# Kernel optimization log

Hardware: AMD Instinct MI355X
Metric: run time of the kernel (lower is better)

The kernel has to match this reference:

```python
import jax, jax.numpy as jnp
import numpy as np

B, S, D = 2, 2048, 1024
H, DH = 16, 64          # n_heads, size_per_head; H*DH == D
FF = 4096               # hidden_dim
EPS = 1e-6              # flax LayerNorm default


def _layernorm(x, scale, bias):
    mu = jnp.mean(x, axis=-1, keepdims=True)
    var = jnp.mean(jnp.square(x - mu), axis=-1, keepdims=True)
    return (x - mu) * jax.lax.rsqrt(var + EPS) * scale + bias


def setup_inputs() -> dict:
    key = jax.random.key(0)
    ks = jax.random.split(key, 12)
    p = lambda k, shape: (jax.random.normal(k, shape, dtype=jnp.float32) * 0.02)
    return {
        "X": jax.random.normal(ks[0], (B, S, D), dtype=jnp.float32),
        "mask": jax.random.randint(ks[1], (B, S), 0, 2, dtype=jnp.int32),
        "Wq": p(ks[2], (D, H * DH)), "bq": jnp.zeros((H * DH,), jnp.float32),
        "Wk": p(ks[3], (D, H * DH)), "bk": jnp.zeros((H * DH,), jnp.float32),
        "Wv": p(ks[4], (D, H * DH)), "bv": jnp.zeros((H * DH,), jnp.float32),
        "Wo": p(ks[5], (H * DH, D)), "bo": jnp.zeros((D,), jnp.float32),
        "ln0_scale": jnp.ones((D,), jnp.float32), "ln0_bias": jnp.zeros((D,), jnp.float32),
        "W1": p(ks[6], (D, FF)), "b1": jnp.zeros((FF,), jnp.float32),
        "W2": p(ks[7], (FF, D)), "b2": jnp.zeros((D,), jnp.float32),
        "ln1_scale": jnp.ones((D,), jnp.float32), "ln1_bias": jnp.zeros((D,), jnp.float32),
    }


def reference(X, mask, Wq, bq, Wk, bk, Wv, bv, Wo, bo,
              ln0_scale, ln0_bias, W1, b1, W2, b2, ln1_scale, ln1_bias):
    b, n, d = X.shape

    def proj(x, W, bias):
        # (B,S,D) -> (B,H,S,DH)
        return (x @ W + bias).reshape(b, n, H, DH).swapaxes(1, 2)

    q = proj(X, Wq, bq)
    k = proj(X, Wk, bk)
    v = proj(X, Wv, bv)

    # scaled dot-product attention with additive padding mask
    scores = jnp.einsum('bhnd,bhmd->bhnm', q, k) / jnp.sqrt(jnp.asarray(DH, X.dtype))
    m = mask[:, None, None, :].astype(scores.dtype)  # (B,1,1,M)
    scores = scores + m * -10000.0
    attn = jax.nn.softmax(scores, axis=-1)
    out = jnp.einsum('bhnm,bhmd->bhnd', attn, v)      # (B,H,S,DH)
    out = out.swapaxes(1, 2).reshape(b, n, H * DH)
    out = out @ Wo + bo

    # add & norm
    X1 = _layernorm(X + out, ln0_scale, ln0_bias)

    # feed-forward
    ff = jnp.maximum(X1 @ W1 + b1, 0.0) @ W2 + b2

    # add & norm
    return _layernorm(X1 + ff, ln1_scale, ln1_bias)
```

## Files before the change

### kernel.cpp

```cpp
#include <hip/hip_runtime.h>
#include <hip/hip_bf16.h>
#include <stdint.h>

#define B_ 2
#define S_ 2048
#define D_ 1024
#define H_ 16
#define DH_ 64
#define FF_ 4096
#define M_ (B_*S_)

typedef __bf16 bf16;
typedef __bf16 bf16x4 __attribute__((ext_vector_type(4)));
typedef __bf16 bf16x8 __attribute__((ext_vector_type(8)));
typedef float f32x4 __attribute__((ext_vector_type(4)));

#define LOG2E 1.44269504f

__device__ __forceinline__ float fexp2(float x) {
#if __has_builtin(__builtin_amdgcn_exp2f)
  return __builtin_amdgcn_exp2f(x);
#else
  return exp2f(x);
#endif
}

__device__ __forceinline__ void gload_lds16(const void* g, void* l) {
  auto gp = reinterpret_cast<const __attribute__((address_space(1))) void*>(
      reinterpret_cast<uintptr_t>(g));
  auto lp = reinterpret_cast<__attribute__((address_space(3))) void*>(
      reinterpret_cast<uintptr_t>(l));
  __builtin_amdgcn_global_load_lds(gp, lp, 16, 0, 0);
}

__global__ __launch_bounds__(256) void prep_all(
    const float* __restrict__ X, bf16* __restrict__ Xb,
    const float* __restrict__ bq, const float* __restrict__ bk,
    const float* __restrict__ bv, float* __restrict__ bqkv,
    const int* __restrict__ mask, float* __restrict__ Mp,
    const float* __restrict__ Wq, const float* __restrict__ Wk,
    const float* __restrict__ Wv, const float* __restrict__ Wo,
    const float* __restrict__ W1, const float* __restrict__ W2,
    bf16* __restrict__ Wqkvt, bf16* __restrict__ Wot,
    bf16* __restrict__ W1t, bf16* __restrict__ W2t) {
  int bid = blockIdx.x;
  const int tid = threadIdx.x;
  if (bid < 4096) {
    int i = (bid * 256 + tid) * 4;
    float4 v = *(const float4*)(X + i);
    Xb[i+0] = (bf16)v.x; Xb[i+1] = (bf16)v.y;
    Xb[i+2] = (bf16)v.z; Xb[i+3] = (bf16)v.w;
    return;
  }
  bid -= 4096;
  if (bid < 12) {
    int i = bid * 256 + tid;
    bqkv[i] = i < 1024 ? bq[i] : (i < 2048 ? bk[i-1024] : bv[i-2048]);
    return;
  }
  bid -= 12;
  if (bid < 16) {
    int i = bid * 256 + tid;
    Mp[i] = (-10000.0f * LOG2E) * (float)mask[i];
    return;
  }
  bid -= 16;
  const float* src; bf16* dst; int K, N;
  if (bid < 1024)      { src = Wq; dst = Wqkvt;                     K=1024; N=1024; }
  else if (bid < 2048) { src = Wk; dst = Wqkvt + (size_t)1024*1024; K=1024; N=1024; bid -= 1024; }
  else if (bid < 3072) { src = Wv; dst = Wqkvt + (size_t)2048*1024; K=1024; N=1024; bid -= 2048; }
  else if (bid < 4096) { src = Wo; dst = Wot;                       K=1024; N=1024; bid -= 3072; }
  else if (bid < 8192) { src = W1; dst = W1t;                       K=1024; N=4096; bid -= 4096; }
  else                 { src = W2; dst = W2t;                       K=4096; N=1024; bid -= 8192; }
  __shared__ float t[32][33];
  const int tx = tid & 31, ty = tid >> 5;
  const int nt32 = N >> 5;
  const int n0 = (bid % nt32) * 32, k0 = (bid / nt32) * 32;
#pragma unroll
  for (int i = 0; i < 4; i++)
    t[ty + i*8][tx] = src[(size_t)(k0 + ty + i*8) * N + n0 + tx];
  __syncthreads();
#pragma unroll
  for (int i = 0; i < 4; i++)
    dst[(size_t)(n0 + ty + i*8) * K + k0 + tx] = (bf16)t[tx][ty + i*8];
}
#define PREP_BLOCKS (4096 + 12 + 16 + 4*1024 + 2*4096)

__global__ __launch_bounds__(256) void transpose_v(
    const bf16* __restrict__ QKV, bf16* __restrict__ Vt) {
  __shared__ bf16 t[64][66];
  int bh = blockIdx.x, s0 = blockIdx.y * 64;
  int b = bh >> 4, h = bh & 15;
  int w = threadIdx.x >> 6, l = threadIdx.x & 63;
#pragma unroll
  for (int i = 0; i < 16; i++) {
    int sr = w*16 + i;
    t[sr][l] = QKV[(size_t)(b*S_ + s0 + sr) * 3072 + 2*D_ + h*DH_ + l];
  }
  __syncthreads();
  const int pcol = (l & 15) * 4 + (l >> 4);
#pragma unroll
  for (int i = 0; i < 16; i++) {
    int dh = w*16 + i;
    Vt[((size_t)(bh*DH_ + dh)) * S_ + s0 + pcol] = t[l][dh];
  }
}

template<int SK>
__global__ __launch_bounds__(256) void gemm_sk(
    const bf16* __restrict__ A, const bf16* __restrict__ Bt,
    const float* __restrict__ bias, float* __restrict__ Cp,
    int M, int N, int K) {
  __shared__ bf16 As[2][128*64];
  __shared__ bf16 Bs[2][128*64];
  const int tid = threadIdx.x;
  const int w = tid >> 6, l = tid & 63;
  const int wm = w >> 1, wn = w & 1;
  const int r16 = l & 15, g = l >> 4;

  const int gx = gridDim.x, gxy = gx * gridDim.y;
  const int nwg = gxy * SK;
  const int lid = (blockIdx.z * gridDim.y + blockIdx.y) * gx + blockIdx.x;
  const int swz = (lid & 7) * (nwg >> 3) + (lid >> 3);
  const int z = swz / gxy, rem = swz % gxy;
  const int m0 = (rem / gx) * 128, n0 = (rem % gx) * 128;
  const int kc = K / SK, kb = z * kc;

  const int srow = w*8 + (l >> 3);
  const int sch  = ((l & 7) ^ (l >> 3)) * 8;
  const bf16* ag = A + (size_t)(m0 + srow) * K + kb + sch;
  const bf16* bg = Bt + (size_t)(n0 + srow) * K + kb + sch;

  f32x4 acc[4][4];
#pragma unroll
  for (int i = 0; i < 4; i++)
#pragma unroll
    for (int j = 0; j < 4; j++) acc[i][j] = (f32x4){0.f,0.f,0.f,0.f};

#pragma unroll
  for (int q = 0; q < 4; q++) {
    gload_lds16(ag + (size_t)(q*32) * K, &As[0][(q*32 + w*8) * 64]);
    gload_lds16(bg + (size_t)(q*32) * K, &Bs[0][(q*32 + w*8) * 64]);
  }
  asm volatile("s_waitcnt vmcnt(0)" ::: "memory");
  __builtin_amdgcn_s_barrier();
  asm volatile("" ::: "memory");

  const int nt = kc >> 6;
  int cur = 0;
  for (int t = 0; t < nt; ++t) {
    if (t + 1 < nt) {
      const int k0 = (t + 1) * 64;
#pragma unroll
      for (int q = 0; q < 4; q++) {
        gload_lds16(ag + (size_t)(q*32) * K + k0, &As[cur^1][(q*32 + w*8) * 64]);
        gload_lds16(bg + (size_t)(q*32) * K + k0, &Bs[cur^1][(q*32 + w*8) * 64]);
      }
    }
    bf16x8 af[4][2], bfr[4][2];
#pragma unroll
    for (int mi = 0; mi < 4; mi++)
#pragma unroll
      for (int kk = 0; kk < 2; kk++) {
        const int row = wm*64 + mi*16 + r16;
        af[mi][kk] = *(const bf16x8*)&As[cur][row*64 + (((kk*4+g) ^ (row & 7)))*8];
      }
#pragma unroll
    for (int ni = 0; ni < 4; ni++)
#pragma unroll
      for (int kk = 0; kk < 2; kk++) {
        const int row = wn*64 + ni*16 + r16;
        bfr[ni][kk] = *(const bf16x8*)&Bs[cur][row*64 + (((kk*4+g) ^ (row & 7)))*8];
      }
    __builtin_amdgcn_s_setprio(1);
#pragma unroll
    for (int mi = 0; mi < 4; mi++)
#pragma unroll
      for (int ni = 0; ni < 4; ni++)
#pragma unroll
        for (int kk = 0; kk < 2; kk++)
          acc[mi][ni] = __builtin_amdgcn_mfma_f32_16x16x32_bf16(
              af[mi][kk], bfr[ni][kk], acc[mi][ni], 0, 0, 0);
    __builtin_amdgcn_s_setprio(0);

    asm volatile("s_waitcnt vmcnt(0)" ::: "memory");
    __builtin_amdgcn_s_barrier();
    asm volatile("" ::: "memory");
    cur ^= 1;
  }

  float* outp = Cp + (size_t)z * M * N;
  float bvs[4];
#pragma unroll
  for (int ni = 0; ni < 4; ni++)
    bvs[ni] = (z == 0) ? bias[n0 + wn*64 + ni*16 + r16] : 0.f;
#pragma unroll
  for (int mi = 0; mi < 4; mi++)
#pragma unroll
    for (int ni = 0; ni < 4; ni++)
#pragma unroll
      for (int r = 0; r < 4; r++) {
        size_t row = (size_t)(m0 + wm*64 + mi*16 + g*4 + r);
        size_t col = (size_t)(n0 + wn*64 + ni*16 + r16);
        outp[row * N + col] = acc[mi][ni][r] + bvs[ni];
      }
}

template<bool RELU>
__global__ __launch_bounds__(512) void gemm256(
    const bf16* __restrict__ A, const bf16* __restrict__ Bt,
    const float* __restrict__ bias, bf16* __restrict__ C,
    int M, int N, int K) {
  __shared__ bf16 As[2][256*64];
  __shared__ bf16 Bs[2][256*64];
  const int tid = threadIdx.x;
  const int w = tid >> 6, l = tid & 63;
  const int wm = w >> 2, wn = w & 3;
  const int r16 = l & 15, g = l >> 4;

  const int gx = gridDim.x;
  const int nwg = gx * gridDim.y;
  const int lid = blockIdx.y * gx + blockIdx.x;
  const int swz = (lid & 7) * (nwg >> 3) + (lid >> 3);
  const int m0 = (swz / gx) * 256, n0 = (swz % gx) * 256;

  const int srow = w*8 + (l >> 3);
  const int sch  = ((l & 7) ^ (l >> 3)) * 8;
  const bf16* ag = A  + (size_t)(m0 + srow) * K + sch;
  const bf16* bg = Bt + (size_t)(n0 + srow) * K + sch;

  f32x4 acc[8][4];
#pragma unroll
  for (int i = 0; i < 8; i++)
#pragma unroll
    for (int j = 0; j < 4; j++) acc[i][j] = (f32x4){0.f,0.f,0.f,0.f};

#pragma unroll
  for (int q = 0; q < 4; q++) {
    gload_lds16(ag + (size_t)(q*64) * K, &As[0][(q*64 + w*8) * 64]);
    gload_lds16(bg + (size_t)(q*64) * K, &Bs[0][(q*64 + w*8) * 64]);
  }
  asm volatile("s_waitcnt vmcnt(0)" ::: "memory");
  __builtin_amdgcn_s_barrier();
  asm volatile("" ::: "memory");

  const int nt = K >> 6;
  int cur = 0;
  for (int t = 0; t < nt; ++t) {
    if (t + 1 < nt) {
      const size_t k0 = (size_t)(t + 1) << 6;
#pragma unroll
      for (int q = 0; q < 4; q++) {
        gload_lds16(ag + (size_t)(q*64) * K + k0, &As[cur^1][(q*64 + w*8) * 64]);
        gload_lds16(bg + (size_t)(q*64) * K + k0, &Bs[cur^1][(q*64 + w*8) * 64]);
      }
    }

    bf16x8 af[4][2], blo[2][2], bhi[2][2];
#pragma unroll
    for (int mi = 0; mi < 4; mi++)
#pragma unroll
      for (int kk = 0; kk < 2; kk++) {
        const int row = wm*128 + mi*16 + r16;
        af[mi][kk] = *(const bf16x8*)&As[cur][row*64 + (((kk*4+g) ^ (row & 7)))*8];
      }
#pragma unroll
    for (int ni = 0; ni < 2; ni++)
#pragma unroll
      for (int kk = 0; kk < 2; kk++) {
        const int row = wn*64 + ni*16 + r16;
        blo[ni][kk] = *(const bf16x8*)&Bs[cur][row*64 + (((kk*4+g) ^ (row & 7)))*8];
      }
    __builtin_amdgcn_s_setprio(1);
#pragma unroll
    for (int mi = 0; mi < 4; mi++)
#pragma unroll
      for (int ni = 0; ni < 2; ni++)
#pragma unroll
        for (int kk = 0; kk < 2; kk++)
          acc[mi][ni] = __builtin_amdgcn_mfma_f32_16x16x32_bf16(
              af[mi][kk], blo[ni][kk], acc[mi][ni], 0, 0, 0);
    __builtin_amdgcn_s_setprio(0);
#pragma unroll
    for (int ni = 0; ni < 2; ni++)
#pragma unroll
      for (int kk = 0; kk < 2; kk++) {
        const int row = wn*64 + 32 + ni*16 + r16;
        bhi[ni][kk] = *(const bf16x8*)&Bs[cur][row*64 + (((kk*4+g) ^ (row & 7)))*8];
      }
    __builtin_amdgcn_s_setprio(1);
#pragma unroll
    for (int mi = 0; mi < 4; mi++)
#pragma unroll
      for (int ni = 0; ni < 2; ni++)
#pragma unroll
        for (int kk = 0; kk < 2; kk++)
          acc[mi][2+ni] = __builtin_amdgcn_mfma_f32_16x16x32_bf16(
              af[mi][kk], bhi[ni][kk], acc[mi][2+ni], 0, 0, 0);
    __builtin_amdgcn_s_setprio(0);
#pragma unroll
    for (int mi = 0; mi < 4; mi++)
#pragma unroll
      for (int kk = 0; kk < 2; kk++) {
        const int row = wm*128 + 64 + mi*16 + r16;
        af[mi][kk] = *(const bf16x8*)&As[cur][row*64 + (((kk*4+g) ^ (row & 7)))*8];
      }
    __builtin_amdgcn_s_setprio(1);
#pragma unroll
    for (int mi = 0; mi < 4; mi++)
#pragma unroll
      for (int ni = 0; ni < 2; ni++)
#pragma unroll
        for (int kk = 0; kk < 2; kk++)
          acc[4+mi][2+ni] = __builtin_amdgcn_mfma_f32_16x16x32_bf16(
              af[mi][kk], bhi[ni][kk], acc[4+mi][2+ni], 0, 0, 0);
    __builtin_amdgcn_s_setprio(0);
    __builtin_amdgcn_s_setprio(1);
#pragma unroll
    for (int mi = 0; mi < 4; mi++)
#pragma unroll
      for (int ni = 0; ni < 2; ni++)
#pragma unroll
        for (int kk = 0; kk < 2; kk++)
          acc[4+mi][ni] = __builtin_amdgcn_mfma_f32_16x16x32_bf16(
              af[mi][kk], blo[ni][kk], acc[4+mi][ni], 0, 0, 0);
    __builtin_amdgcn_s_setprio(0);

    asm volatile("s_waitcnt vmcnt(0)" ::: "memory");
    __builtin_amdgcn_s_barrier();
    asm volatile("" ::: "memory");
    cur ^= 1;
  }

  float bvs[4];
#pragma unroll
  for (int ni = 0; ni < 4; ni++) bvs[ni] = bias[n0 + wn*64 + ni*16 + r16];
#pragma unroll
  for (int mi = 0; mi < 8; mi++)
#pragma unroll
    for (int ni = 0; ni < 4; ni++)
#pragma unroll
      for (int r = 0; r < 4; r++) {
        float v = acc[mi][ni][r] + bvs[ni];
        if (RELU) v = fmaxf(v, 0.f);
        C[(size_t)(m0 + wm*128 + mi*16 + g*4 + r) * N +
          (n0 + wn*64 + ni*16 + r16)] = (bf16)v;
      }
}

__global__ __launch_bounds__(256) void attn(
    const bf16* __restrict__ QKV, const bf16* __restrict__ Vt,
    const float* __restrict__ Mp, bf16* __restrict__ AO) {
  __shared__ bf16 Ks[2][64*64];
  __shared__ bf16 Vs[2][64*64];
  __shared__ bf16 Ps[4][32*72];

  const float SC2 = 0.125f * LOG2E;
  const int bh = blockIdx.x, b = bh >> 4, h = bh & 15;
  const int q0 = blockIdx.y * 128;
  const int tid = threadIdx.x, w = tid >> 6, l = tid & 63;
  const int r16 = l & 15, g = l >> 4;
  const int qw = q0 + w*32;

  bf16x8 qf[2][2];
#pragma unroll
  for (int s = 0; s < 2; s++)
#pragma unroll
    for (int kk = 0; kk < 2; kk++)
      qf[s][kk] = *(const bf16x8*)&QKV[((size_t)(b*S_ + qw + s*16 + r16))*3072
                                       + h*64 + kk*32 + g*8];

  const int srow = w*8 + (l >> 3);
  const int sch  = (l & 7) ^ (l >> 3);
  const bf16* kg = QKV + ((size_t)(b*S_) + srow)*3072 + 1024 + h*64 + sch*8;
  const bf16* vg = Vt + ((size_t)(bh*64 + srow))*S_ + sch*8;

  f32x4 po[2][4];
#pragma unroll
  for (int s = 0; s < 2; s++)
#pragma unroll
    for (int n = 0; n < 4; n++) po[s][n] = (f32x4){0.f,0.f,0.f,0.f};
  float mrun[8], lsum[8];
#pragma unroll
  for (int r = 0; r < 8; r++) { mrun[r] = -1.0e30f; lsum[r] = 0.f; }

  float madd[4];
#pragma unroll
  for (int ct = 0; ct < 4; ct++) madd[ct] = Mp[b*S_ + ct*16 + r16];
#pragma unroll
  for (int p = 0; p < 2; p++) {
    gload_lds16(kg + (size_t)(p*32)*3072, &Ks[0][(p*256 + w*64)*8]);
    gload_lds16(vg + (size_t)(p*32)*S_,   &Vs[0][(p*256 + w*64)*8]);
  }

  const int NT = S_/64;
  int cur = 0;
  for (int it = 0; it < NT; ++it) {
    const int kv0 = it * 64;
    if (it + 1 < NT) {
#pragma unroll
      for (int p = 0; p < 2; p++) {
        gload_lds16(kg + (size_t)(kv0 + 64 + p*32)*3072, &Ks[cur^1][(p*256 + w*64)*8]);
        gload_lds16(vg + (size_t)(p*32)*S_ + (kv0 + 64), &Vs[cur^1][(p*256 + w*64)*8]);
      }
      asm volatile("s_waitcnt vmcnt(4)" ::: "memory");
    } else {
      asm volatile("s_waitcnt vmcnt(0)" ::: "memory");
    }
    __builtin_amdgcn_s_barrier();
    asm volatile("" ::: "memory");

    float sv[2][4][4];
    __builtin_amdgcn_s_setprio(1);
#pragma unroll
    for (int ct = 0; ct < 4; ct++) {
      const int row = ct*16 + r16;
      bf16x8 kf0 = *(const bf16x8*)&Ks[cur][row*64 + ((g) ^ (row & 7))*8];
      bf16x8 kf1 = *(const bf16x8*)&Ks[cur][row*64 + ((4+g) ^ (row & 7))*8];
      f32x4 a0 = (f32x4){0.f,0.f,0.f,0.f}, a1 = (f32x4){0.f,0.f,0.f,0.f};
      a0 = __builtin_amdgcn_mfma_f32_16x16x32_bf16(qf[0][0], kf0, a0, 0, 0, 0);
      a0 = __builtin_amdgcn_mfma_f32_16x16x32_bf16(qf[0][1], kf1, a0, 0, 0, 0);
      a1 = __builtin_amdgcn_mfma_f32_16x16x32_bf16(qf[1][0], kf0, a1, 0, 0, 0);
      a1 = __builtin_amdgcn_mfma_f32_16x16x32_bf16(qf[1][1], kf1, a1, 0, 0, 0);
#pragma unroll
      for (int r = 0; r < 4; r++) {
        sv[0][ct][r] = a0[r]*SC2 + madd[ct];
        sv[1][ct][r] = a1[r]*SC2 + madd[ct];
      }
    }
    __builtin_amdgcn_s_setprio(0);

    if (it + 1 < NT) {
#pragma unroll
      for (int ct = 0; ct < 4; ct++)
        madd[ct] = Mp[b*S_ + kv0 + 64 + ct*16 + r16];
    }

    float lmax[8];
#pragma unroll
    for (int s = 0; s < 2; s++)
#pragma unroll
      for (int r = 0; r < 4; r++)
        lmax[s*4+r] = fmaxf(fmaxf(sv[s][0][r], sv[s][1][r]),
                            fmaxf(sv[s][2][r], sv[s][3][r]));
    bool grow = false;
#pragma unroll
    for (int i = 0; i < 8; i++) grow |= (lmax[i] > mrun[i] + 8.f);
    if (__any(grow)) {
#pragma unroll
      for (int s = 0; s < 2; s++)
#pragma unroll
        for (int r = 0; r < 4; r++) {
          const int i = s*4 + r;
          float t = lmax[i];
#pragma unroll
          for (int off = 8; off >= 1; off >>= 1) t = fmaxf(t, __shfl_xor(t, off, 16));
          float mnew = fmaxf(mrun[i], t);
          float sc = fexp2(mrun[i] - mnew);
          mrun[i] = mnew;
          lsum[i] *= sc;
#pragma unroll
          for (int n = 0; n < 4; n++) po[s][n][r] *= sc;
        }
    }
#pragma unroll
    for (int s = 0; s < 2; s++)
#pragma unroll
      for (int r = 0; r < 4; r++) {
        const int i = s*4 + r;
#pragma unroll
        for (int ct = 0; ct < 4; ct++)
          sv[s][ct][r] = fexp2(sv[s][ct][r] - mrun[i]);
        lsum[i] += (sv[s][0][r] + sv[s][1][r]) + (sv[s][2][r] + sv[s][3][r]);
      }

#pragma unroll
    for (int s = 0; s < 2; s++)
#pragma unroll
      for (int r = 0; r < 4; r++) {
        bf16x4 pk;
#pragma unroll
        for (int ct = 0; ct < 4; ct++) pk[ct] = (bf16)sv[s][ct][r];
        *(bf16x4*)&Ps[w][(s*16 + g*4 + r)*72 + r16*4] = pk;
      }
    asm volatile("s_waitcnt lgkmcnt(0)" ::: "memory");

    __builtin_amdgcn_s_setprio(1);
#pragma unroll
    for (int kk = 0; kk < 2; kk++) {
      bf16x8 pa0 = *(const bf16x8*)&Ps[w][(r16)*72 + kk*32 + g*8];
      bf16x8 pa1 = *(const bf16x8*)&Ps[w][(16 + r16)*72 + kk*32 + g*8];
#pragma unroll
      for (int n = 0; n < 4; n++) {
        const int row = n*16 + r16;
        bf16x8 vf = *(const bf16x8*)&Vs[cur][row*64 + ((kk*4 + g) ^ (row & 7))*8];
        po[0][n] = __builtin_amdgcn_mfma_f32_16x16x32_bf16(pa0, vf, po[0][n], 0, 0, 0);
        po[1][n] = __builtin_amdgcn_mfma_f32_16x16x32_bf16(pa1, vf, po[1][n], 0, 0, 0);
      }
    }
    __builtin_amdgcn_s_setprio(0);

    __builtin_amdgcn_s_barrier();
    asm volatile("" ::: "memory");
    cur ^= 1;
  }

#pragma unroll
  for (int i = 0; i < 8; i++) {
    float t = lsum[i];
#pragma unroll
    for (int off = 8; off >= 1; off >>= 1) t += __shfl_xor(t, off, 16);
    lsum[i] = t;
  }

#pragma unroll
  for (int s = 0; s < 2; s++)
#pragma unroll
    for (int n = 0; n < 4; n++)
#pragma unroll
      for (int r = 0; r < 4; r++) {
        float v = po[s][n][r] / lsum[s*4 + r];
        AO[(size_t)(b*S_ + qw + s*16 + g*4 + r)*D_ + h*64 + n*16 + r16] = (bf16)v;
      }
}

template<bool XF32, bool OUTF32>
__global__ __launch_bounds__(256) void ln_res2(
    const void* __restrict__ xp, const float* __restrict__ p0,
    const float* __restrict__ p1, const float* __restrict__ sc,
    const float* __restrict__ bi, float* __restrict__ y,
    bf16* __restrict__ yb) {
  const int row = blockIdx.x, tid = threadIdx.x;
  const size_t base = (size_t)row * D_;
  float v[4];
  if (XF32) {
    float4 a = ((const float4*)((const float*)xp + base))[tid];
    v[0] = a.x; v[1] = a.y; v[2] = a.z; v[3] = a.w;
  } else {
    bf16x4 a = *(const bf16x4*)&((const bf16*)xp)[base + tid*4];
#pragma unroll
    for (int j = 0; j < 4; j++) v[j] = (float)a[j];
  }
  float4 a0 = ((const float4*)(p0 + base))[tid];
  float4 a1 = ((const float4*)(p1 + base))[tid];
  v[0] += a0.x + a1.x; v[1] += a0.y + a1.y;
  v[2] += a0.z + a1.z; v[3] += a0.w + a1.w;
  float s  = v[0] + v[1] + v[2] + v[3];
  float ss = v[0]*v[0] + v[1]*v[1] + v[2]*v[2] + v[3]*v[3];
#pragma unroll
  for (int off = 32; off >= 1; off >>= 1) {
    s  += __shfl_xor(s, off, 64);
    ss += __shfl_xor(ss, off, 64);
  }
  __shared__ float red[8];
  const int wv = tid >> 6;
  if ((tid & 63) == 0) { red[wv] = s; red[4 + wv] = ss; }
  __syncthreads();
  s  = red[0] + red[1] + red[2] + red[3];
  ss = red[4] + red[5] + red[6] + red[7];
  const float mu  = s * (1.0f / D_);
  const float inv = rsqrtf(ss * (1.0f / D_) - mu*mu + 1e-6f);
  float4 scv = ((const float4*)sc)[tid];
  float4 biv = ((const float4*)bi)[tid];
  float o[4];
  o[0] = (v[0]-mu)*inv*scv.x + biv.x;
  o[1] = (v[1]-mu)*inv*scv.y + biv.y;
  o[2] = (v[2]-mu)*inv*scv.z + biv.z;
  o[3] = (v[3]-mu)*inv*scv.w + biv.w;
  if (OUTF32) {
    ((float4*)(y + base))[tid] = make_float4(o[0], o[1], o[2], o[3]);
  } else {
    bf16x4 ob;
#pragma unroll
    for (int j = 0; j < 4; j++) ob[j] = (bf16)o[j];
    *(bf16x4*)&yb[base + tid*4] = ob;
  }
}

extern "C" void kernel_launch(void* const* d_in, const int* in_sizes, int n_in,
                              void* d_out, int out_size, void* d_ws, size_t ws_size,
                              hipStream_t stream) {
  const float* X    = (const float*)d_in[0];
  const int*   mask = (const int*)d_in[1];
  const float* Wq   = (const float*)d_in[2];
  const float* bq   = (const float*)d_in[3];
  const float* Wk   = (const float*)d_in[4];
  const float* bk   = (const float*)d_in[5];
  const float* Wv   = (const float*)d_in[6];
  const float* bv   = (const float*)d_in[7];
  const float* Wo   = (const float*)d_in[8];
  const float* bo   = (const float*)d_in[9];
  const float* ln0s = (const float*)d_in[10];
  const float* ln0b = (const float*)d_in[11];
  const float* W1   = (const float*)d_in[12];
  const float* b1   = (const float*)d_in[13];
  const float* W2   = (const float*)d_in[14];
  const float* b2   = (const float*)d_in[15];
  const float* ln1s = (const float*)d_in[16];
  const float* ln1b = (const float*)d_in[17];
  float* out = (float*)d_out;

  char* ws = (char*)d_ws;
  const size_t MB = 1024 * 1024;
  bf16*  Xb    = (bf16*)(ws + 0);
  bf16*  X1b   = (bf16*)(ws + 0);
  bf16*  Wqkvt = (bf16*)(ws + 8*MB);
  bf16*  Wot   = (bf16*)(ws + 14*MB);
  bf16*  W1t   = (bf16*)(ws + 16*MB);
  bf16*  W2t   = (bf16*)(ws + 24*MB);
  bf16*  QKV   = (bf16*)(ws + 32*MB);
  bf16*  AO    = (bf16*)(ws + 32*MB);
  bf16*  Vt    = (bf16*)(ws + 56*MB);
  bf16*  FF1   = (bf16*)(ws + 32*MB);
  float* P0    = (float*)(ws + 64*MB);
  float* P1    = (float*)(ws + 80*MB);
  float* bqkv  = (float*)(ws + 64*MB);
  float* Mp    = (float*)(ws + 64*MB + 16384);

  prep_all<<<PREP_BLOCKS, 256, 0, stream>>>(
      X, Xb, bq, bk, bv, bqkv, mask, Mp,
      Wq, Wk, Wv, Wo, W1, W2, Wqkvt, Wot, W1t, W2t);

  gemm256<false><<<dim3(3072/256, M_/256), 512, 0, stream>>>(Xb, Wqkvt, bqkv, QKV, M_, 3072, D_);
  transpose_v<<<dim3(32, S_/64), 256, 0, stream>>>(QKV, Vt);
  attn<<<dim3(32, S_/128), 256, 0, stream>>>(QKV, Vt, Mp, AO);
  gemm_sk<2><<<dim3(D_/128, M_/128, 2), 256, 0, stream>>>(AO, Wot, bo, P0, M_, D_, D_);
  ln_res2<false,false><<<M_, 256, 0, stream>>>(Xb, P0, P1, ln0s, ln0b, nullptr, X1b);
  gemm256<true><<<dim3(FF_/256, M_/256), 512, 0, stream>>>(X1b, W1t, b1, FF1, M_, FF_, D_);
  gemm_sk<2><<<dim3(D_/128, M_/128, 2), 256, 0, stream>>>(FF1, W2t, b2, P0, M_, D_, FF_);
  ln_res2<false,true><<<M_, 256, 0, stream>>>(X1b, P0, P1, ln1s, ln1b, out, nullptr);
}
```

Baseline: 228.6 us.

## Split attention block into 8 waves of 16 query rows each

The attention kernel now launches 512 threads per block, with 8 waves each owning 16 query rows instead of 4 waves owning 32. K/V tile loads are spread over 8 waves, so each thread issues one load per tile instead of two. This is meant to raise wave-level parallelism and latency hiding and to cut per-wave registers. In exchange each wave reuses every K/V LDS fragment for only one MFMA, which doubles LDS read traffic per FLOP and adds barrier participants.

```diff
diff --git a/kernel.cpp b/kernel.cpp
--- a/kernel.cpp
+++ b/kernel.cpp
@@ -348,85 +348,70 @@
       }
 }
 
-__global__ __launch_bounds__(256) void attn(
+__global__ __launch_bounds__(512) void attn(
     const bf16* __restrict__ QKV, const bf16* __restrict__ Vt,
     const float* __restrict__ Mp, bf16* __restrict__ AO) {
   __shared__ bf16 Ks[2][64*64];
   __shared__ bf16 Vs[2][64*64];
-  __shared__ bf16 Ps[4][32*72];
+  __shared__ bf16 Ps[8][16*72];
 
   const float SC2 = 0.125f * LOG2E;
   const int bh = blockIdx.x, b = bh >> 4, h = bh & 15;
   const int q0 = blockIdx.y * 128;
   const int tid = threadIdx.x, w = tid >> 6, l = tid & 63;
   const int r16 = l & 15, g = l >> 4;
-  const int qw = q0 + w*32;
-
-  bf16x8 qf[2][2];
-#pragma unroll
-  for (int s = 0; s < 2; s++)
-#pragma unroll
-    for (int kk = 0; kk < 2; kk++)
-      qf[s][kk] = *(const bf16x8*)&QKV[((size_t)(b*S_ + qw + s*16 + r16))*3072
-                                       + h*64 + kk*32 + g*8];
+  const int qw = q0 + w*16;
+
+  bf16x8 qf[2];
+#pragma unroll
+  for (int kk = 0; kk < 2; kk++)
+    qf[kk] = *(const bf16x8*)&QKV[((size_t)(b*S_ + qw + r16))*3072
+                                  + h*64 + kk*32 + g*8];
 
   const int srow = w*8 + (l >> 3);
   const int sch  = (l & 7) ^ (l >> 3);
   const bf16* kg = QKV + ((size_t)(b*S_) + srow)*3072 + 1024 + h*64 + sch*8;
   const bf16* vg = Vt + ((size_t)(bh*64 + srow))*S_ + sch*8;
 
-  f32x4 po[2][4];
-#pragma unroll
-  for (int s = 0; s < 2; s++)
-#pragma unroll
-    for (int n = 0; n < 4; n++) po[s][n] = (f32x4){0.f,0.f,0.f,0.f};
-  float mrun[8], lsum[8];
-#pragma unroll
-  for (int r = 0; r < 8; r++) { mrun[r] = -1.0e30f; lsum[r] = 0.f; }
+  f32x4 po[4];
+#pragma unroll
+  for (int n = 0; n < 4; n++) po[n] = (f32x4){0.f,0.f,0.f,0.f};
+  float mrun[4], lsum[4];
+#pragma unroll
+  for (int r = 0; r < 4; r++) { mrun[r] = -1.0e30f; lsum[r] = 0.f; }
 
   float madd[4];
 #pragma unroll
   for (int ct = 0; ct < 4; ct++) madd[ct] = Mp[b*S_ + ct*16 + r16];
-#pragma unroll
-  for (int p = 0; p < 2; p++) {
-    gload_lds16(kg + (size_t)(p*32)*3072, &Ks[0][(p*256 + w*64)*8]);
-    gload_lds16(vg + (size_t)(p*32)*S_,   &Vs[0][(p*256 + w*64)*8]);
-  }
+  gload_lds16(kg, &Ks[0][w*512]);
+  gload_lds16(vg, &Vs[0][w*512]);
 
   const int NT = S_/64;
   int cur = 0;
   for (int it = 0; it < NT; ++it) {
     const int kv0 = it * 64;
     if (it + 1 < NT) {
-#pragma unroll
-      for (int p = 0; p < 2; p++) {
-        gload_lds16(kg + (size_t)(kv0 + 64 + p*32)*3072, &Ks[cur^1][(p*256 + w*64)*8]);
-        gload_lds16(vg + (size_t)(p*32)*S_ + (kv0 + 64), &Vs[cur^1][(p*256 + w*64)*8]);
-      }
-      asm volatile("s_waitcnt vmcnt(4)" ::: "memory");
+      gload_lds16(kg + (size_t)(kv0 + 64)*3072, &Ks[cur^1][w*512]);
+      gload_lds16(vg + kv0 + 64,                &Vs[cur^1][w*512]);
+      asm volatile("s_waitcnt vmcnt(2)" ::: "memory");
     } else {
       asm volatile("s_waitcnt vmcnt(0)" ::: "memory");
     }
     __builtin_amdgcn_s_barrier();
     asm volatile("" ::: "memory");
 
-    float sv[2][4][4];
+    float sv[4][4];
     __builtin_amdgcn_s_setprio(1);
 #pragma unroll
     for (int ct = 0; ct < 4; ct++) {
       const int row = ct*16 + r16;
       bf16x8 kf0 = *(const bf16x8*)&Ks[cur][row*64 + ((g) ^ (row & 7))*8];
       bf16x8 kf1 = *(const bf16x8*)&Ks[cur][row*64 + ((4+g) ^ (row & 7))*8];
-      f32x4 a0 = (f32x4){0.f,0.f,0.f,0.f}, a1 = (f32x4){0.f,0.f,0.f,0.f};
-      a0 = __builtin_amdgcn_mfma_f32_16x16x32_bf16(qf[0][0], kf0, a0, 0, 0, 0);
-      a0 = __builtin_amdgcn_mfma_f32_16x16x32_bf16(qf[0][1], kf1, a0, 0, 0, 0);
-      a1 = __builtin_amdgcn_mfma_f32_16x16x32_bf16(qf[1][0], kf0, a1, 0, 0, 0);
-      a1 = __builtin_amdgcn_mfma_f32_16x16x32_bf16(qf[1][1], kf1, a1, 0, 0, 0);
-#pragma unroll
-      for (int r = 0; r < 4; r++) {
-        sv[0][ct][r] = a0[r]*SC2 + madd[ct];
-        sv[1][ct][r] = a1[r]*SC2 + madd[ct];
-      }
+      f32x4 s = (f32x4){0.f,0.f,0.f,0.f};
+      s = __builtin_amdgcn_mfma_f32_16x16x32_bf16(qf[0], kf0, s, 0, 0, 0);
+      s = __builtin_amdgcn_mfma_f32_16x16x32_bf16(qf[1], kf1, s, 0, 0, 0);
+#pragma unroll
+      for (int r = 0; r < 4; r++) sv[ct][r] = s[r]*SC2 + madd[ct];
     }
     __builtin_amdgcn_s_setprio(0);
 
@@ -436,66 +421,52 @@
         madd[ct] = Mp[b*S_ + kv0 + 64 + ct*16 + r16];
     }
 
-    float lmax[8];
-#pragma unroll
-    for (int s = 0; s < 2; s++)
-#pragma unroll
-      for (int r = 0; r < 4; r++)
-        lmax[s*4+r] = fmaxf(fmaxf(sv[s][0][r], sv[s][1][r]),
-                            fmaxf(sv[s][2][r], sv[s][3][r]));
-    bool grow = false;
-#pragma unroll
-    for (int i = 0; i < 8; i++) grow |= (lmax[i] > mrun[i] + 8.f);
+    float lmax[4];
+#pragma unroll
+    for (int r = 0; r < 4; r++)
+      lmax[r] = fmaxf(fmaxf(sv[0][r], sv[1][r]), fmaxf(sv[2][r], sv[3][r]));
+    bool grow = (lmax[0] > mrun[0] + 8.f) | (lmax[1] > mrun[1] + 8.f) |
+                (lmax[2] > mrun[2] + 8.f) | (lmax[3] > mrun[3] + 8.f);
     if (__any(grow)) {
 #pragma unroll
-      for (int s = 0; s < 2; s++)
-#pragma unroll
-        for (int r = 0; r < 4; r++) {
-          const int i = s*4 + r;
-          float t = lmax[i];
-#pragma unroll
-          for (int off = 8; off >= 1; off >>= 1) t = fmaxf(t, __shfl_xor(t, off, 16));
-          float mnew = fmaxf(mrun[i], t);
-          float sc = fexp2(mrun[i] - mnew);
-          mrun[i] = mnew;
-          lsum[i] *= sc;
-#pragma unroll
-          for (int n = 0; n < 4; n++) po[s][n][r] *= sc;
-        }
-    }
-#pragma unroll
-    for (int s = 0; s < 2; s++)
-#pragma unroll
       for (int r = 0; r < 4; r++) {
-        const int i = s*4 + r;
-#pragma unroll
-        for (int ct = 0; ct < 4; ct++)
-          sv[s][ct][r] = fexp2(sv[s][ct][r] - mrun[i]);
-        lsum[i] += (sv[s][0][r] + sv[s][1][r]) + (sv[s][2][r] + sv[s][3][r]);
-      }
-
-#pragma unroll
-    for (int s = 0; s < 2; s++)
-#pragma unroll
-      for (int r = 0; r < 4; r++) {
-        bf16x4 pk;
-#pragma unroll
-        for (int ct = 0; ct < 4; ct++) pk[ct] = (bf16)sv[s][ct][r];
-        *(bf16x4*)&Ps[w][(s*16 + g*4 + r)*72 + r16*4] = pk;
-      }
+        float t = lmax[r];
+#pragma unroll
+        for (int off = 8; off >= 1; off >>= 1) t = fmaxf(t, __shfl_xor(t, off, 16));
+        float mnew = fmaxf(mrun[r], t);
+        float sc = fexp2(mrun[r] - mnew);
+        mrun[r] = mnew;
+        lsum[r] *= sc;
+#pragma unroll
+        for (int n = 0; n < 4; n++) po[n][r] *= sc;
+      }
+    }
+#pragma unroll
+    for (int r = 0; r < 4; r++) {
+#pragma unroll
+      for (int ct = 0; ct < 4; ct++)
+        sv[ct][r] = fexp2(sv[ct][r] - mrun[r]);
+      lsum[r] += (sv[0][r] + sv[1][r]) + (sv[2][r] + sv[3][r]);
+    }
+
+#pragma unroll
+    for (int r = 0; r < 4; r++) {
+      bf16x4 pk;
+#pragma unroll
+      for (int ct = 0; ct < 4; ct++) pk[ct] = (bf16)sv[ct][r];
+      *(bf16x4*)&Ps[w][(g*4 + r)*72 + r16*4] = pk;
+    }
     asm volatile("s_waitcnt lgkmcnt(0)" ::: "memory");
 
     __builtin_amdgcn_s_setprio(1);
 #pragma unroll
     for (int kk = 0; kk < 2; kk++) {
-      bf16x8 pa0 = *(const bf16x8*)&Ps[w][(r16)*72 + kk*32 + g*8];
-      bf16x8 pa1 = *(const bf16x8*)&Ps[w][(16 + r16)*72 + kk*32 + g*8];
+      bf16x8 pa = *(const bf16x8*)&Ps[w][r16*72 + kk*32 + g*8];
 #pragma unroll
       for (int n = 0; n < 4; n++) {
         const int row = n*16 + r16;
         bf16x8 vf = *(const bf16x8*)&Vs[cur][row*64 + ((kk*4 + g) ^ (row & 7))*8];
-        po[0][n] = __builtin_amdgcn_mfma_f32_16x16x32_bf16(pa0, vf, po[0][n], 0, 0, 0);
-        po[1][n] = __builtin_amdgcn_mfma_f32_16x16x32_bf16(pa1, vf, po[1][n], 0, 0, 0);
+        po[n] = __builtin_amdgcn_mfma_f32_16x16x32_bf16(pa, vf, po[n], 0, 0, 0);
       }
     }
     __builtin_amdgcn_s_setprio(0);
@@ -506,22 +477,20 @@
   }
 
 #pragma unroll
-  for (int i = 0; i < 8; i++) {
-    float t = lsum[i];
+  for (int r = 0; r < 4; r++) {
+    float t = lsum[r];
 #pragma unroll
     for (int off = 8; off >= 1; off >>= 1) t += __shfl_xor(t, off, 16);
-    lsum[i] = t;
-  }
-
-#pragma unroll
-  for (int s = 0; s < 2; s++)
-#pragma unroll
-    for (int n = 0; n < 4; n++)
-#pragma unroll
-      for (int r = 0; r < 4; r++) {
-        float v = po[s][n][r] / lsum[s*4 + r];
-        AO[(size_t)(b*S_ + qw + s*16 + g*4 + r)*D_ + h*64 + n*16 + r16] = (bf16)v;
-      }
+    lsum[r] = t;
+  }
+
+#pragma unroll
+  for (int n = 0; n < 4; n++)
+#pragma unroll
+    for (int r = 0; r < 4; r++) {
+      float v = po[n][r] / lsum[r];
+      AO[(size_t)(b*S_ + qw + g*4 + r)*D_ + h*64 + n*16 + r16] = (bf16)v;
+    }
 }
 
 template<bool XF32, bool OUTF32>
@@ -623,7 +592,7 @@
 
   gemm256<false><<<dim3(3072/256, M_/256), 512, 0, stream>>>(Xb, Wqkvt, bqkv, QKV, M_, 3072, D_);
   transpose_v<<<dim3(32, S_/64), 256, 0, stream>>>(QKV, Vt);
-  attn<<<dim3(32, S_/128), 256, 0, stream>>>(QKV, Vt, Mp, AO);
+  attn<<<dim3(32, S_/128), 512, 0, stream>>>(QKV, Vt, Mp, AO);
   gemm_sk<2><<<dim3(D_/128, M_/128, 2), 256, 0, stream>>>(AO, Wot, bo, P0, M_, D_, D_);
   ln_res2<false,false><<<M_, 256, 0, stream>>>(Xb, P0, P1, ln0s, ln0b, nullptr, X1b);
   gemm256<true><<<dim3(FF_/256, M_/256), 512, 0, stream>>>(X1b, W1t, b1, FF1, M_, FF_, D_);
```

Result: faster. 218.4 us (median of 2 runs) (-4.5%).
